# Kernel tuning notes

Hardware: AMD Instinct MI355X
Metric: run time of the kernel (lower is better)

## Reference

```python
import jax, jax.numpy as jnp
import numpy as np

N_EMBD = 384
N_HEAD = 6
HEAD_SIZE = N_EMBD // N_HEAD  # 64
B, T, S = 128, 256, 256
EPS = 1e-5


def setup_inputs() -> dict:
    key = jax.random.key(0)
    ks = jax.random.split(key, 20)
    w = lambda k, shape: (jax.random.normal(k, shape, dtype=jnp.float32) * 0.02)
    inp = {
        'x': jax.random.normal(ks[0], (B, T, N_EMBD), dtype=jnp.float32),
        'encoder_output': jax.random.normal(ks[1], (B, S, N_EMBD), dtype=jnp.float32),
        # masked self-attention heads (stacked over heads): [H, C, D]
        'wq1': w(ks[2], (N_HEAD, N_EMBD, HEAD_SIZE)),
        'wk1': w(ks[3], (N_HEAD, N_EMBD, HEAD_SIZE)),
        'wv1': w(ks[4], (N_HEAD, N_EMBD, HEAD_SIZE)),
        'proj1_w': w(ks[5], (N_EMBD, N_EMBD)),
        'proj1_b': jnp.zeros((N_EMBD,), jnp.float32),
        # cross-attention heads
        'wq2': w(ks[6], (N_HEAD, N_EMBD, HEAD_SIZE)),
        'wk2': w(ks[7], (N_HEAD, N_EMBD, HEAD_SIZE)),
        'wv2': w(ks[8], (N_HEAD, N_EMBD, HEAD_SIZE)),
        'proj2_w': w(ks[9], (N_EMBD, N_EMBD)),
        'proj2_b': jnp.zeros((N_EMBD,), jnp.float32),
        # feed-forward
        'ffn_w1': w(ks[10], (N_EMBD, 4 * N_EMBD)),
        'ffn_b1': jnp.zeros((4 * N_EMBD,), jnp.float32),
        'ffn_w2': w(ks[11], (4 * N_EMBD, N_EMBD)),
        'ffn_b2': jnp.zeros((N_EMBD,), jnp.float32),
        # layernorms
        'ln1_g': jnp.ones((N_EMBD,), jnp.float32), 'ln1_b': jnp.zeros((N_EMBD,), jnp.float32),
        'ln2_g': jnp.ones((N_EMBD,), jnp.float32), 'ln2_b': jnp.zeros((N_EMBD,), jnp.float32),
        'ln3_g': jnp.ones((N_EMBD,), jnp.float32), 'ln3_b': jnp.zeros((N_EMBD,), jnp.float32),
    }
    return inp


def _layernorm(x, g, b):
    mu = jnp.mean(x, axis=-1, keepdims=True)
    var = jnp.mean(jnp.square(x - mu), axis=-1, keepdims=True)
    return (x - mu) * jax.lax.rsqrt(var + EPS) * g + b


def _mha(xq, xkv, wq, wk, wv, proj_w, proj_b, causal):
    # NOTE: source scales by C**-0.5 with C = n_embd (not head_size)
    scale = jnp.asarray(N_EMBD, xq.dtype) ** -0.5
    q = jnp.einsum('btc,hcd->bhtd', xq, wq)
    k = jnp.einsum('bsc,hcd->bhsd', xkv, wk)
    v = jnp.einsum('bsc,hcd->bhsd', xkv, wv)
    wei = jnp.einsum('bhtd,bhsd->bhts', q, k) * scale
    if causal:
        Tq, Tk = xq.shape[1], xkv.shape[1]
        mask = jnp.tril(jnp.ones((Tq, Tk), dtype=bool))
        wei = jnp.where(mask, wei, jnp.asarray(-jnp.inf, wei.dtype))
    p = jax.nn.softmax(wei, axis=-1)  # dropout omitted (eval mode)
    o = jnp.einsum('bhts,bhsd->bhtd', p, v)
    Bq, H, Tq, D = o.shape
    o = o.transpose(0, 2, 1, 3).reshape(Bq, Tq, H * D)  # concat heads
    return o @ proj_w + proj_b


def reference(x, encoder_output,
              wq1, wk1, wv1, proj1_w, proj1_b,
              wq2, wk2, wv2, proj2_w, proj2_b,
              ffn_w1, ffn_b1, ffn_w2, ffn_b2,
              ln1_g, ln1_b, ln2_g, ln2_b, ln3_g, ln3_b):
    # x = x + masked self-attn(ln1(x))
    x = x + _mha(_layernorm(x, ln1_g, ln1_b), _layernorm(x, ln1_g, ln1_b),
                 wq1, wk1, wv1, proj1_w, proj1_b, causal=True)
    # x = x + cross-attn(ln2(x), encoder_output)  (no mask)
    x = x + _mha(_layernorm(x, ln2_g, ln2_b), encoder_output,
                 wq2, wk2, wv2, proj2_w, proj2_b, causal=False)
    # x = x + ffwd(ln3(x))
    h = _layernorm(x, ln3_g, ln3_b)
    x = x + (jax.nn.relu(h @ ffn_w1 + ffn_b1) @ ffn_w2 + ffn_b2)
    return x
```

## Files before the change

kernel.cpp:

```cpp
#include <hip/hip_runtime.h>
#include <hip/hip_bf16.h>

#define BB 128
#define TT 256
#define CC 384
#define HH 6
#define DD 64
#define NTOK 32768

typedef __attribute__((ext_vector_type(8))) short short8;
typedef __attribute__((ext_vector_type(4))) float f32x4;

__device__ __forceinline__ unsigned short f2bf(float f) {
  union { float f; unsigned int u; } v; v.f = f;
  unsigned int r = v.u + 0x7fff + ((v.u >> 16) & 1);
  return (unsigned short)(r >> 16);
}

__device__ __forceinline__ void glds16(const void* g, void* l) {
  __builtin_amdgcn_global_load_lds((const __attribute__((address_space(1))) void*)g,
                                   (__attribute__((address_space(3))) void*)l, 16, 0, 0);
}

__global__ __launch_bounds__(256) void pack_all_k(
    const float* __restrict__ wq1, const float* __restrict__ wk1, const float* __restrict__ wv1,
    const float* __restrict__ wq2, const float* __restrict__ wk2, const float* __restrict__ wv2,
    const float* __restrict__ proj1_w, const float* __restrict__ proj2_w,
    const float* __restrict__ ffn_w1, const float* __restrict__ ffn_w2,
    unsigned short* __restrict__ W) {
  int idx = blockIdx.x * 256 + threadIdx.x;
  if (idx < 589824) {
    int sub = idx / 147456, r = idx - sub * 147456;
    const float* src = sub == 0 ? wq1 : sub == 1 ? wk1 : sub == 2 ? wv1 : wq2;
    unsigned short* dst = W + sub * 147456;
    int h = r / 24576, rem = r - h * 24576;
    int c = rem >> 6, d = rem & 63;
    dst[(h * 64 + d) * 384 + c] = f2bf(src[r]);
  } else if (idx < 884736) {
    int t = idx - 589824;
    int sub = t / 147456, r = t - sub * 147456;
    const float* src = sub ? wv2 : wk2;
    unsigned short* dst = W + 589824 + sub * 147456;
    int h = r / 24576, rem = r - h * 24576;
    int c = rem >> 6, d = rem & 63;
    dst[(h * 64 + d) * 384 + c] = f2bf(src[r]);
  } else if (idx < 1179648) {
    int t = idx - 884736;
    int sub = t / 147456, r = t - sub * 147456;
    const float* src = sub ? proj2_w : proj1_w;
    unsigned short* dst = W + 884736 + sub * 147456;
    int c = r / 384, n = r - c * 384;
    dst[n * 384 + c] = f2bf(src[r]);
  } else if (idx < 1769472) {
    int r = idx - 1179648;
    int c = r / 1536, n = r - c * 1536;
    (W + 1179648)[n * 384 + c] = f2bf(ffn_w1[r]);
  } else {
    int r = idx - 1769472;
    int c = r / 384, n = r - c * 384;
    (W + 1769472)[n * 1536 + c] = f2bf(ffn_w2[r]);
  }
}

__global__ __launch_bounds__(256) void ln_k(const float* __restrict__ x,
                                            unsigned short* __restrict__ out,
                                            const float* __restrict__ gamma,
                                            const float* __restrict__ beta) {
  int row = blockIdx.x * 4 + (threadIdx.x >> 6);
  int lane = threadIdx.x & 63;
  const float* xr = x + (size_t)row * CC;
  float v[6];
  float s = 0.f;
#pragma unroll
  for (int j = 0; j < 6; ++j) { v[j] = xr[j * 64 + lane]; s += v[j]; }
#pragma unroll
  for (int m = 1; m < 64; m <<= 1) s += __shfl_xor(s, m);
  float mu = s * (1.0f / CC);
  float vs = 0.f;
#pragma unroll
  for (int j = 0; j < 6; ++j) { float d = v[j] - mu; vs += d * d; }
#pragma unroll
  for (int m = 1; m < 64; m <<= 1) vs += __shfl_xor(vs, m);
  float rs = rsqrtf(vs * (1.0f / CC) + 1e-5f);
  unsigned short* orow = out + (size_t)row * CC;
#pragma unroll
  for (int j = 0; j < 6; ++j) {
    int cidx = j * 64 + lane;
    orow[cidx] = f2bf((v[j] - mu) * rs * gamma[cidx] + beta[cidx]);
  }
}

template <int EPI, bool AF32>
__global__ __launch_bounds__(256) void gemm_k(const void* __restrict__ Ap, int lda,
                                              const unsigned short* __restrict__ Bt, int ldb,
                                              void* __restrict__ Cp, int ldc,
                                              const float* __restrict__ bias,
                                              const float* __restrict__ res, int ldres,
                                              int K, int nx) {
  __shared__ unsigned short sA[128 * 64];
  __shared__ unsigned short sB[128 * 64];
  const int tid = threadIdx.x;
  const int chunkg = gridDim.x >> 3;
  const int wg = blockIdx.x;
  const int lg = (wg & 7) * chunkg + (wg >> 3);
  const int bx = lg % nx, by = lg / nx;
  const int m0 = by * 128;
  const int n0 = bx * 128;
  const int wid = tid >> 6, lane = tid & 63;
  const int wr = wid >> 1, wc = wid & 1;
  const int g = lane >> 4, c = lane & 15;

  f32x4 acc[4][4] = {};

  for (int k0 = 0; k0 < K; k0 += 64) {
    if constexpr (!AF32) {
#pragma unroll
      for (int t = 0; t < 4; ++t) {
        int chunk = t * 256 + tid;
        int row = chunk >> 3, grp = chunk & 7;
        const unsigned short* Ab = (const unsigned short*)Ap;
        glds16(&Ab[(size_t)(m0 + row) * lda + k0 + ((grp ^ (row & 7)) << 3)], &sA[chunk * 8]);
      }
    } else {
#pragma unroll
      for (int t = 0; t < 4; ++t) {
        int chunk = t * 256 + tid;
        int row = chunk >> 3, grp = chunk & 7;
        int dst = row * 64 + ((grp ^ (row & 7)) << 3);
        const float* Af = (const float*)Ap + (size_t)(m0 + row) * lda + k0 + grp * 8;
        float4 f0 = *(const float4*)Af;
        float4 f1 = *(const float4*)(Af + 4);
        union { unsigned short h[8]; uint4 u; } t2;
        t2.h[0] = f2bf(f0.x); t2.h[1] = f2bf(f0.y); t2.h[2] = f2bf(f0.z); t2.h[3] = f2bf(f0.w);
        t2.h[4] = f2bf(f1.x); t2.h[5] = f2bf(f1.y); t2.h[6] = f2bf(f1.z); t2.h[7] = f2bf(f1.w);
        *(uint4*)&sA[dst] = t2.u;
      }
    }
#pragma unroll
    for (int t = 0; t < 4; ++t) {
      int chunk = t * 256 + tid;
      int row = chunk >> 3, grp = chunk & 7;
      glds16(&Bt[(size_t)(n0 + row) * ldb + k0 + ((grp ^ (row & 7)) << 3)], &sB[chunk * 8]);
    }
    __syncthreads();
#pragma unroll
    for (int kk = 0; kk < 2; ++kk) {
      short8 a[4], b[4];
#pragma unroll
      for (int mi = 0; mi < 4; ++mi) {
        int r = wr * 64 + mi * 16 + c;
        a[mi] = *(const short8*)&sA[r * 64 + (((kk * 4 + g) ^ (r & 7)) << 3)];
      }
#pragma unroll
      for (int ni = 0; ni < 4; ++ni) {
        int rb = wc * 64 + ni * 16 + c;
        b[ni] = *(const short8*)&sB[rb * 64 + (((kk * 4 + g) ^ (rb & 7)) << 3)];
      }
#pragma unroll
      for (int mi = 0; mi < 4; ++mi)
#pragma unroll
        for (int ni = 0; ni < 4; ++ni)
          acc[mi][ni] = __builtin_amdgcn_mfma_f32_16x16x32_bf16(a[mi], b[ni], acc[mi][ni], 0, 0, 0);
    }
    __syncthreads();
  }

#pragma unroll
  for (int mi = 0; mi < 4; ++mi) {
#pragma unroll
    for (int ni = 0; ni < 4; ++ni) {
#pragma unroll
      for (int i = 0; i < 4; ++i) {
        int row = m0 + wr * 64 + mi * 16 + g * 4 + i;
        int col = n0 + wc * 64 + ni * 16 + c;
        float v = acc[mi][ni][i];
        if (EPI == 0) {
          ((unsigned short*)Cp)[(size_t)row * ldc + col] = f2bf(v);
        } else if (EPI == 1) {
          v += bias[col];
          ((unsigned short*)Cp)[(size_t)row * ldc + col] = f2bf(fmaxf(v, 0.f));
        } else {
          v += bias[col] + res[(size_t)row * ldres + col];
          ((float*)Cp)[(size_t)row * ldc + col] = v;
        }
      }
    }
  }
}

__device__ __forceinline__ int vt_off(int d, int sgrp) {
  return d * 256 + ((((sgrp + (d >> 3)) & 31) ^ (d & 7)) << 3);
}

template <bool CAUSAL>
__global__ __launch_bounds__(512, 2) void attn_k(const unsigned short* __restrict__ QKV,
                                                 unsigned short* __restrict__ O) {
  __shared__ unsigned short Ks[256 * 64];
  __shared__ unsigned short Vt[64 * 256];
  __shared__ unsigned short Ps[8][16 * 40];
  const int bh = blockIdx.x >> 1;
  const int half = blockIdx.x & 1;
  const int b = bh / HH, hh = bh - b * HH;
  const int tid = threadIdx.x, wid = tid >> 6, lane = tid & 63;
  const int g = lane >> 4, c = lane & 15;
  const unsigned short* base = QKV + (size_t)b * TT * 1152;

#pragma unroll
  for (int t = 0; t < 4; ++t) {
    int chunk = t * 512 + tid;
    int s = chunk >> 3, grp = chunk & 7;
    *(uint4*)&Ks[s * 64 + ((grp ^ (s & 7)) << 3)] =
        *(const uint4*)&base[(size_t)s * 1152 + 384 + hh * 64 + grp * 8];
    union { unsigned short h[8]; uint4 u; } tv;
    tv.u = *(const uint4*)&base[(size_t)s * 1152 + 768 + hh * 64 + grp * 8];
#pragma unroll
    for (int j = 0; j < 8; ++j) Vt[vt_off(grp * 8 + j, s >> 3) + (s & 7)] = tv.h[j];
  }
  __syncthreads();

  const float scale = 0.05103103630798287f;
  unsigned short* Pw = &Ps[wid][0];
  const int qr0 = half * 128 + wid * 16;

  short8 aq[2];
#pragma unroll
  for (int kk = 0; kk < 2; ++kk)
    aq[kk] = *(const short8*)&QKV[(size_t)(b * TT + qr0 + c) * 1152 + hh * 64 + kk * 32 + g * 8];

  f32x4 sacc[16] = {};
#pragma unroll
  for (int sj = 0; sj < 16; ++sj) {
    if (!CAUSAL || sj * 16 <= qr0) {
      int rk = sj * 16 + c;
      f32x4 z = sacc[sj];
      z = __builtin_amdgcn_mfma_f32_16x16x32_bf16(
          aq[0], *(const short8*)&Ks[rk * 64 + ((g ^ (rk & 7)) << 3)], z, 0, 0, 0);
      z = __builtin_amdgcn_mfma_f32_16x16x32_bf16(
          aq[1], *(const short8*)&Ks[rk * 64 + (((4 + g) ^ (rk & 7)) << 3)], z, 0, 0, 0);
      sacc[sj] = z;
    }
  }

  float inv[4];
#pragma unroll
  for (int i = 0; i < 4; ++i) {
    const int qr = qr0 + g * 4 + i;
    float mx = -1e30f;
#pragma unroll
    for (int sj = 0; sj < 16; ++sj) {
      if (!CAUSAL || sj * 16 <= qr0) {
        int s = sj * 16 + c;
        float v = sacc[sj][i] * scale;
        if (CAUSAL && s > qr) v = -1e30f;
        sacc[sj][i] = v;
        mx = fmaxf(mx, v);
      }
    }
#pragma unroll
    for (int m = 1; m < 16; m <<= 1) mx = fmaxf(mx, __shfl_xor(mx, m));
    float sum = 0.f;
#pragma unroll
    for (int sj = 0; sj < 16; ++sj) {
      if (!CAUSAL || sj * 16 <= qr0) {
        float p = __expf(sacc[sj][i] - mx);
        sacc[sj][i] = p;
        sum += p;
      }
    }
#pragma unroll
    for (int m = 1; m < 16; m <<= 1) sum += __shfl_xor(sum, m);
    inv[i] = 1.0f / sum;
  }

  f32x4 oacc[4] = {};
#pragma unroll
  for (int sk = 0; sk < 8; ++sk) {
    if (!CAUSAL || sk * 32 <= qr0) {
#pragma unroll
      for (int half_sj = 0; half_sj < 2; ++half_sj) {
        int sj = sk * 2 + half_sj;
#pragma unroll
        for (int i = 0; i < 4; ++i)
          Pw[(g * 4 + i) * 40 + half_sj * 16 + c] = f2bf(sacc[sj][i]);
      }
      short8 ap = *(const short8*)&Pw[c * 40 + g * 8];
#pragma unroll
      for (int dj = 0; dj < 4; ++dj) {
        short8 bv = *(const short8*)&Vt[vt_off(dj * 16 + c, sk * 4 + g)];
        oacc[dj] = __builtin_amdgcn_mfma_f32_16x16x32_bf16(ap, bv, oacc[dj], 0, 0, 0);
      }
    }
  }

#pragma unroll
  for (int dj = 0; dj < 4; ++dj)
#pragma unroll
    for (int i = 0; i < 4; ++i) {
      int qr = qr0 + g * 4 + i;
      O[(size_t)(b * TT + qr) * CC + hh * 64 + dj * 16 + c] = f2bf(oacc[dj][i] * inv[i]);
    }
}

extern "C" void kernel_launch(void* const* d_in, const int* in_sizes, int n_in,
                              void* d_out, int out_size, void* d_ws, size_t ws_size,
                              hipStream_t stream) {
  const float* x = (const float*)d_in[0];
  const float* enc = (const float*)d_in[1];
  const float* wq1 = (const float*)d_in[2];
  const float* wk1 = (const float*)d_in[3];
  const float* wv1 = (const float*)d_in[4];
  const float* proj1_w = (const float*)d_in[5];
  const float* proj1_b = (const float*)d_in[6];
  const float* wq2 = (const float*)d_in[7];
  const float* wk2 = (const float*)d_in[8];
  const float* wv2 = (const float*)d_in[9];
  const float* proj2_w = (const float*)d_in[10];
  const float* proj2_b = (const float*)d_in[11];
  const float* ffn_w1 = (const float*)d_in[12];
  const float* ffn_b1 = (const float*)d_in[13];
  const float* ffn_w2 = (const float*)d_in[14];
  const float* ffn_b2 = (const float*)d_in[15];
  const float* ln1_g = (const float*)d_in[16];
  const float* ln1_b = (const float*)d_in[17];
  const float* ln2_g = (const float*)d_in[18];
  const float* ln2_b = (const float*)d_in[19];
  const float* ln3_g = (const float*)d_in[20];
  const float* ln3_b = (const float*)d_in[21];
  float* out = (float*)d_out;

  char* ws = (char*)d_ws;
  const size_t OFF_A = 0;
  const size_t OFF_X = 50331648;
  const size_t OFF_Q = 75497472;
  const size_t OFF_O = 150994944;
  const size_t OFF_W = 176160768;

  float* xc = (float*)(ws + OFF_A);
  unsigned short* xn = (unsigned short*)(ws + OFF_X);
  unsigned short* qkv = (unsigned short*)(ws + OFF_Q);
  unsigned short* h1 = (unsigned short*)(ws + OFF_Q);
  unsigned short* obuf = (unsigned short*)(ws + OFF_O);
  unsigned short* W = (unsigned short*)(ws + OFF_W);

  unsigned short* Wqkv1t = W + 0;
  unsigned short* Wq2t = W + 442368;
  unsigned short* Wkv2t = W + 589824;
  unsigned short* proj1t = W + 884736;
  unsigned short* proj2t = W + 1032192;
  unsigned short* W1t = W + 1179648;
  unsigned short* W2t = W + 1769472;

  pack_all_k<<<9216, 256, 0, stream>>>(wq1, wk1, wv1, wq2, wk2, wv2,
                                       proj1_w, proj2_w, ffn_w1, ffn_w2, W);

  dim3 blk(256);
  ln_k<<<8192, blk, 0, stream>>>(x, xn, ln1_g, ln1_b);
  gemm_k<0, false><<<2304, blk, 0, stream>>>(xn, 384, Wqkv1t, 384, qkv, 1152,
                                             nullptr, nullptr, 0, 384, 9);
  attn_k<true><<<1536, 512, 0, stream>>>(qkv, obuf);
  gemm_k<2, false><<<768, blk, 0, stream>>>(obuf, 384, proj1t, 384, xc, 384,
                                            proj1_b, x, 384, 384, 3);
  ln_k<<<8192, blk, 0, stream>>>(xc, xn, ln2_g, ln2_b);
  gemm_k<0, false><<<768, blk, 0, stream>>>(xn, 384, Wq2t, 384, qkv, 1152,
                                            nullptr, nullptr, 0, 384, 3);
  gemm_k<0, true><<<1536, blk, 0, stream>>>(enc, 384, Wkv2t, 384, qkv + 384, 1152,
                                            nullptr, nullptr, 0, 384, 6);
  attn_k<false><<<1536, 512, 0, stream>>>(qkv, obuf);
  gemm_k<2, false><<<768, blk, 0, stream>>>(obuf, 384, proj2t, 384, xc, 384,
                                            proj2_b, xc, 384, 384, 3);
  ln_k<<<8192, blk, 0, stream>>>(xc, xn, ln3_g, ln3_b);
  gemm_k<1, false><<<3072, blk, 0, stream>>>(xn, 384, W1t, 384, h1, 1536,
                                             ffn_b1, nullptr, 0, 384, 12);
  gemm_k<2, false><<<768, blk, 0, stream>>>(h1, 1536, W2t, 1536, out, 384,
                                            ffn_b2, xc, 384, 1536, 3);
}
```

Measured before the change: 444.7 us.

## Double-buffer GEMM LDS tiles to overlap global loads with MFMA compute

The GEMM kernel now uses two LDS buffers per operand and stages the next K-tile while the MFMAs run on the current one, with one barrier per iteration instead of two. The last iteration prefetches the residual tile and the bias values into registers so the epilogue does not wait on global loads. This hides load latency behind compute, at the cost of doubled LDS use (64KB per block) and extra registers for the residual values, which may limit occupancy.

```diff
diff --git a/kernel.cpp b/kernel.cpp
--- a/kernel.cpp
+++ b/kernel.cpp
@@ -20,6 +20,11 @@
 __device__ __forceinline__ void glds16(const void* g, void* l) {
   __builtin_amdgcn_global_load_lds((const __attribute__((address_space(1))) void*)g,
                                    (__attribute__((address_space(3))) void*)l, 16, 0, 0);
+}
+
+__device__ __forceinline__ void vm_drain() {
+  asm volatile("s_waitcnt vmcnt(0)" ::: "memory");
+  __builtin_amdgcn_sched_barrier(0);
 }
 
 __global__ __launch_bounds__(256) void pack_all_k(
@@ -90,15 +95,76 @@
   }
 }
 
+template <bool AF32>
+__device__ __forceinline__ void stage_tile(const void* Ap, int lda,
+                                           const unsigned short* Bt, int ldb,
+                                           int m0, int n0, int k0, int tid,
+                                           unsigned short* sAb, unsigned short* sBb) {
+  if constexpr (!AF32) {
+#pragma unroll
+    for (int t = 0; t < 4; ++t) {
+      int chunk = t * 256 + tid;
+      int row = chunk >> 3, grp = chunk & 7;
+      const unsigned short* Ab = (const unsigned short*)Ap;
+      glds16(&Ab[(size_t)(m0 + row) * lda + k0 + ((grp ^ (row & 7)) << 3)], &sAb[chunk * 8]);
+    }
+  } else {
+#pragma unroll
+    for (int t = 0; t < 4; ++t) {
+      int chunk = t * 256 + tid;
+      int row = chunk >> 3, grp = chunk & 7;
+      int dst = row * 64 + ((grp ^ (row & 7)) << 3);
+      const float* Af = (const float*)Ap + (size_t)(m0 + row) * lda + k0 + grp * 8;
+      float4 f0 = *(const float4*)Af;
+      float4 f1 = *(const float4*)(Af + 4);
+      union { unsigned short h[8]; uint4 u; } t2;
+      t2.h[0] = f2bf(f0.x); t2.h[1] = f2bf(f0.y); t2.h[2] = f2bf(f0.z); t2.h[3] = f2bf(f0.w);
+      t2.h[4] = f2bf(f1.x); t2.h[5] = f2bf(f1.y); t2.h[6] = f2bf(f1.z); t2.h[7] = f2bf(f1.w);
+      *(uint4*)&sAb[dst] = t2.u;
+    }
+  }
+#pragma unroll
+  for (int t = 0; t < 4; ++t) {
+    int chunk = t * 256 + tid;
+    int row = chunk >> 3, grp = chunk & 7;
+    glds16(&Bt[(size_t)(n0 + row) * ldb + k0 + ((grp ^ (row & 7)) << 3)], &sBb[chunk * 8]);
+  }
+}
+
+__device__ __forceinline__ void compute_tile(const unsigned short* sAb, const unsigned short* sBb,
+                                             int wr, int wc, int g, int c, f32x4 (&acc)[4][4]) {
+#pragma unroll
+  for (int kk = 0; kk < 2; ++kk) {
+    short8 a[4], b[4];
+#pragma unroll
+    for (int mi = 0; mi < 4; ++mi) {
+      int r = wr * 64 + mi * 16 + c;
+      a[mi] = *(const short8*)&sAb[r * 64 + (((kk * 4 + g) ^ (r & 7)) << 3)];
+    }
+#pragma unroll
+    for (int ni = 0; ni < 4; ++ni) {
+      int rb = wc * 64 + ni * 16 + c;
+      b[ni] = *(const short8*)&sBb[rb * 64 + (((kk * 4 + g) ^ (rb & 7)) << 3)];
+    }
+#pragma unroll
+    for (int mi = 0; mi < 4; ++mi)
+#pragma unroll
+      for (int ni = 0; ni < 4; ++ni)
+        acc[mi][ni] = __builtin_amdgcn_mfma_f32_16x16x32_bf16(a[mi], b[ni], acc[mi][ni], 0, 0, 0);
+  }
+}
+
 template <int EPI, bool AF32>
-__global__ __launch_bounds__(256) void gemm_k(const void* __restrict__ Ap, int lda,
-                                              const unsigned short* __restrict__ Bt, int ldb,
-                                              void* __restrict__ Cp, int ldc,
-                                              const float* __restrict__ bias,
-                                              const float* __restrict__ res, int ldres,
-                                              int K, int nx) {
-  __shared__ unsigned short sA[128 * 64];
-  __shared__ unsigned short sB[128 * 64];
+__global__ __launch_bounds__(256, 2) void gemm_k(const void* __restrict__ Ap, int lda,
+                                                 const unsigned short* __restrict__ Bt, int ldb,
+                                                 void* __restrict__ Cp, int ldc,
+                                                 const float* __restrict__ bias,
+                                                 const float* __restrict__ res, int ldres,
+                                                 int K, int nx) {
+  __shared__ unsigned short sA0[128 * 64];
+  __shared__ unsigned short sB0[128 * 64];
+  __shared__ unsigned short sA1[128 * 64];
+  __shared__ unsigned short sB1[128 * 64];
   const int tid = threadIdx.x;
   const int chunkg = gridDim.x >> 3;
   const int wg = blockIdx.x;
@@ -111,59 +177,49 @@
   const int g = lane >> 4, c = lane & 15;
 
   f32x4 acc[4][4] = {};
-
-  for (int k0 = 0; k0 < K; k0 += 64) {
-    if constexpr (!AF32) {
-#pragma unroll
-      for (int t = 0; t < 4; ++t) {
-        int chunk = t * 256 + tid;
-        int row = chunk >> 3, grp = chunk & 7;
-        const unsigned short* Ab = (const unsigned short*)Ap;
-        glds16(&Ab[(size_t)(m0 + row) * lda + k0 + ((grp ^ (row & 7)) << 3)], &sA[chunk * 8]);
-      }
-    } else {
-#pragma unroll
-      for (int t = 0; t < 4; ++t) {
-        int chunk = t * 256 + tid;
-        int row = chunk >> 3, grp = chunk & 7;
-        int dst = row * 64 + ((grp ^ (row & 7)) << 3);
-        const float* Af = (const float*)Ap + (size_t)(m0 + row) * lda + k0 + grp * 8;
-        float4 f0 = *(const float4*)Af;
-        float4 f1 = *(const float4*)(Af + 4);
-        union { unsigned short h[8]; uint4 u; } t2;
-        t2.h[0] = f2bf(f0.x); t2.h[1] = f2bf(f0.y); t2.h[2] = f2bf(f0.z); t2.h[3] = f2bf(f0.w);
-        t2.h[4] = f2bf(f1.x); t2.h[5] = f2bf(f1.y); t2.h[6] = f2bf(f1.z); t2.h[7] = f2bf(f1.w);
-        *(uint4*)&sA[dst] = t2.u;
-      }
-    }
-#pragma unroll
-    for (int t = 0; t < 4; ++t) {
-      int chunk = t * 256 + tid;
-      int row = chunk >> 3, grp = chunk & 7;
-      glds16(&Bt[(size_t)(n0 + row) * ldb + k0 + ((grp ^ (row & 7)) << 3)], &sB[chunk * 8]);
-    }
+  float biasr[4];
+  if (EPI >= 1) {
+#pragma unroll
+    for (int ni = 0; ni < 4; ++ni) biasr[ni] = bias[n0 + wc * 64 + ni * 16 + c];
+  }
+  float resr[4][4][4];
+
+  const int nt = K >> 6;
+
+#define LOAD_RES()                                                                    \
+  do {                                                                                \
+    if (EPI == 2) {                                                                   \
+      _Pragma("unroll") for (int mi = 0; mi < 4; ++mi)                                \
+      _Pragma("unroll") for (int i = 0; i < 4; ++i) {                                 \
+        int row = m0 + wr * 64 + mi * 16 + g * 4 + i;                                 \
+        _Pragma("unroll") for (int ni = 0; ni < 4; ++ni)                              \
+          resr[mi][ni][i] = res[(size_t)row * ldres + n0 + wc * 64 + ni * 16 + c];    \
+      }                                                                               \
+    }                                                                                 \
+  } while (0)
+
+  stage_tile<AF32>(Ap, lda, Bt, ldb, m0, n0, 0, tid, sA0, sB0);
+  vm_drain();
+  __syncthreads();
+
+  int t = 0;
+  for (;;) {
+    if (t + 1 < nt) stage_tile<AF32>(Ap, lda, Bt, ldb, m0, n0, (t + 1) * 64, tid, sA1, sB1);
+    else LOAD_RES();
+    compute_tile(sA0, sB0, wr, wc, g, c, acc);
+    if (t + 1 >= nt) break;
+    vm_drain();
     __syncthreads();
-#pragma unroll
-    for (int kk = 0; kk < 2; ++kk) {
-      short8 a[4], b[4];
-#pragma unroll
-      for (int mi = 0; mi < 4; ++mi) {
-        int r = wr * 64 + mi * 16 + c;
-        a[mi] = *(const short8*)&sA[r * 64 + (((kk * 4 + g) ^ (r & 7)) << 3)];
-      }
-#pragma unroll
-      for (int ni = 0; ni < 4; ++ni) {
-        int rb = wc * 64 + ni * 16 + c;
-        b[ni] = *(const short8*)&sB[rb * 64 + (((kk * 4 + g) ^ (rb & 7)) << 3)];
-      }
-#pragma unroll
-      for (int mi = 0; mi < 4; ++mi)
-#pragma unroll
-        for (int ni = 0; ni < 4; ++ni)
-          acc[mi][ni] = __builtin_amdgcn_mfma_f32_16x16x32_bf16(a[mi], b[ni], acc[mi][ni], 0, 0, 0);
-    }
+    ++t;
+    if (t + 1 < nt) stage_tile<AF32>(Ap, lda, Bt, ldb, m0, n0, (t + 1) * 64, tid, sA0, sB0);
+    else LOAD_RES();
+    compute_tile(sA1, sB1, wr, wc, g, c, acc);
+    if (t + 1 >= nt) break;
+    vm_drain();
     __syncthreads();
-  }
+    ++t;
+  }
+#undef LOAD_RES
 
 #pragma unroll
   for (int mi = 0; mi < 4; ++mi) {
@@ -177,10 +233,10 @@
         if (EPI == 0) {
           ((unsigned short*)Cp)[(size_t)row * ldc + col] = f2bf(v);
         } else if (EPI == 1) {
-          v += bias[col];
+          v += biasr[ni];
           ((unsigned short*)Cp)[(size_t)row * ldc + col] = f2bf(fmaxf(v, 0.f));
         } else {
-          v += bias[col] + res[(size_t)row * ldres + col];
+          v += biasr[ni] + resr[mi][ni][i];
           ((float*)Cp)[(size_t)row * ldc + col] = v;
         }
       }
```

New measurement: 472.3 us. 6.2% more time.
